# Kernel optimization log

Hardware: AMD Instinct MI355X
Metric: run time of the kernel (lower is better)

The kernel has to match this reference:

```python
import jax, jax.numpy as jnp
import numpy as np

USER = 100000
ITEM = 100000
N = USER + ITEM          # total nodes
D = 64                   # latdim
DEG = 16                 # avg edges per user (before symmetrization)
L_GNN = 2                # args.gnn_layer
L_MLP = 2                # args.layer_mlp
EPS = 1e-5               # LayerNorm eps


def setup_inputs() -> dict:
    key = jax.random.key(0)
    k1, k2, k3, k4, k5 = jax.random.split(key, 5)
    # bipartite user->item edges, then symmetrize (bi_adj over N x N nodes)
    u = jax.random.randint(k1, (USER * DEG,), 0, USER)
    v = jax.random.randint(k2, (USER * DEG,), 0, ITEM) + USER
    rows = jnp.concatenate([u, v]).astype(jnp.int64)
    cols = jnp.concatenate([v, u]).astype(jnp.int64)
    # symmetric D^-1/2 A D^-1/2 normalization (matches _normalize_adj)
    deg = jnp.zeros((N,), jnp.float32).at[rows].add(1.0)
    vals = 1.0 / (jnp.sqrt(deg[rows]) * jnp.sqrt(deg[cols]))
    # xavier-uniform-ish initial embeddings (detached in the source)
    bound = float(np.sqrt(6.0 / (N + D)))
    ini_embeds = jax.random.uniform(k3, (N, D), jnp.float32, -bound, bound)
    # MLP params: L_MLP stacked Linear(latdim, latdim)
    wb = float(np.sqrt(6.0 / (D + D)))
    Ws = jax.random.uniform(k4, (L_MLP, D, D), jnp.float32, -wb, wb)
    bs = jnp.zeros((L_MLP, D), jnp.float32)
    gamma = jnp.ones((D,), jnp.float32)
    beta = jnp.zeros((D,), jnp.float32)
    return {"rows": rows, "cols": cols, "vals": vals, "ini_embeds": ini_embeds,
            "Ws": Ws, "bs": bs, "gamma": gamma, "beta": beta}


def reference(rows, cols, vals, ini_embeds, Ws, bs, gamma, beta):
    # UntrainedGCN.forward: multi-hop spmm propagation (concat=0, symetric=True)
    e = ini_embeds
    for _ in range(L_GNN):
        # spmm: out[r] += vals * e[c] for each edge (r, c)
        e = jax.ops.segment_sum(vals[:, None] * e[cols], rows, num_segments=N)
    # residual MLP: relu(Wx+b) + x per FeedForwardLayer
    for i in range(L_MLP):
        e = jax.nn.relu(e @ Ws[i].T + bs[i]) + e
    # LayerNorm over last dim
    mu = e.mean(-1, keepdims=True)
    xc = e - mu
    var = (xc * xc).mean(-1, keepdims=True)
    e = xc * jax.lax.rsqrt(var + EPS) * gamma + beta
    return e[:USER], e[USER:]
```

## Files before the change

### kernel.cpp

```cpp
#include <hip/hip_runtime.h>
#include <hip/hip_bf16.h>

#define NN      200000
#define D       64
#define NTILE   12500
#define BKT_SH  8
#define BKT_RW  256
#define NBKT    782
#define NCHUNK  128
#define L2CAP   6656
#define CPAD    16
#define RSENT   256

typedef __attribute__((ext_vector_type(8))) short short8;
typedef __attribute__((ext_vector_type(4))) float f32x4;

__device__ inline unsigned short f32_to_bf16_rne(float x) {
    unsigned u = __float_as_uint(x);
    unsigned r = u + 0x7FFFu + ((u >> 16) & 1u);
    return (unsigned short)(r >> 16);
}
__device__ inline float bf16_bits_to_f32(unsigned short h) {
    return __uint_as_float(((unsigned)h) << 16);
}
__device__ inline unsigned pack2_bf16_rne(float lo, float hi) {
    unsigned a = __float_as_uint(lo);
    unsigned b = __float_as_uint(hi);
    a = a + 0x7FFFu + ((a >> 16) & 1u);
    b = b + 0x7FFFu + ((b >> 16) & 1u);
    return (a >> 16) | (b & 0xFFFF0000u);
}
__device__ inline float bf_lo(unsigned u) { return __uint_as_float(u << 16); }
__device__ inline float bf_hi(unsigned u) { return __uint_as_float(u & 0xFFFF0000u); }

__global__ __launch_bounds__(256) void zero_f4(float4* __restrict__ p, int n4) {
    int i = blockIdx.x * blockDim.x + threadIdx.x;
    if (i < n4) p[i] = make_float4(0.f, 0.f, 0.f, 0.f);
}
__global__ __launch_bounds__(256) void zero_i(int* __restrict__ p, int n) {
    int i = blockIdx.x * blockDim.x + threadIdx.x;
    if (i < n) p[i] = 0;
}
__global__ __launch_bounds__(256) void cvt_bf16(const float2* __restrict__ in,
                                                unsigned* __restrict__ out, int n) {
    int stride = gridDim.x * blockDim.x;
    for (int i = blockIdx.x * blockDim.x + threadIdx.x; i < n; i += stride) {
        float2 v = in[i];
        out[i] = pack2_bf16_rne(v.x, v.y);
    }
}

template <int ALIGN>
__global__ __launch_bounds__(1024) void bkt_count(const int* __restrict__ rows,
                                                  int* __restrict__ tot_p,
                                                  int E, int epb) {
    __shared__ int h[NBKT];
    int t = threadIdx.x;
    for (int i = t; i < NBKT; i += 1024) h[i] = 0;
    __syncthreads();
    int start = blockIdx.x * epb;
    int end   = min(E, start + epb);
    for (int e = start + t; e < end; e += 1024)
        atomicAdd(&h[rows[e] >> BKT_SH], 1);
    __syncthreads();
    for (int i = t; i < NBKT; i += 1024) {
        int c   = h[i];
        int res = (c + ALIGN - 1) & ~(ALIGN - 1);
        if (res) atomicAdd(&tot_p[i * CPAD], res);
    }
}

__global__ __launch_bounds__(1024) void bkt_scan(const int* __restrict__ tot_p,
                                                 int* __restrict__ bktstart,
                                                 int* __restrict__ cursor_p) {
    __shared__ int s[1024];
    int t = threadIdx.x;
    int v = (t < NBKT) ? tot_p[t * CPAD] : 0;
    s[t] = v;
    __syncthreads();
    #pragma unroll
    for (int d = 1; d < 1024; d <<= 1) {
        int a = (t >= d) ? s[t - d] : 0;
        __syncthreads();
        s[t] += a;
        __syncthreads();
    }
    if (t < NBKT) {
        int ex = s[t] - v;
        bktstart[t] = ex;
        cursor_p[t * CPAD] = ex;
    }
    if (t == 0) bktstart[NBKT] = s[1023];
}

template <int ALIGN>
__global__ __launch_bounds__(1024) void scatter_l1(const int* __restrict__ rows,
                                                   const int* __restrict__ cols,
                                                   const float* __restrict__ vals,
                                                   int* __restrict__ cursor_p,
                                                   int2* __restrict__ packed,
                                                   int E, int epb) {
    __shared__ int h[NBKT];
    __shared__ int base[NBKT];
    int t = threadIdx.x;
    for (int i = t; i < NBKT; i += 1024) h[i] = 0;
    __syncthreads();
    int start = blockIdx.x * epb;
    int end   = min(E, start + epb);
    for (int e = start + t; e < end; e += 1024)
        atomicAdd(&h[rows[e] >> BKT_SH], 1);
    __syncthreads();
    for (int i = t; i < NBKT; i += 1024) {
        int c   = h[i];
        int res = (c + ALIGN - 1) & ~(ALIGN - 1);
        int b0  = res ? atomicAdd(&cursor_p[i * CPAD], res) : 0;
        base[i] = b0;
        for (int j = c; j < res; ++j)
            packed[b0 + j] = make_int2(RSENT << 18, 0);
        h[i] = 0;
    }
    __syncthreads();
    for (int e = start + t; e < end; e += 1024) {
        int r = rows[e];
        int b = r >> BKT_SH;
        int p = base[b] + atomicAdd(&h[b], 1);
        packed[p] = make_int2(cols[e] | ((r & (BKT_RW - 1)) << 18),
                              __float_as_int(vals[e]));
    }
}

__global__ __launch_bounds__(256) void sort_l2(const int* __restrict__ bktstart,
                                               int2* __restrict__ packed,
                                               int* __restrict__ rp,
                                               int* __restrict__ rpe) {
    __shared__ int2 sm[L2CAP];
    __shared__ int  cnt[BKT_RW];
    __shared__ int  cur[BKT_RW];
    int b = blockIdx.x;
    int s = bktstart[b];
    int e = bktstart[b + 1];
    int n = e - s;
    if (n > L2CAP) n = L2CAP;
    int t = threadIdx.x;
    cnt[t] = 0;
    __syncthreads();
    for (int i = t; i < n; i += 256) {
        int2 v = packed[s + i];
        sm[i] = v;
        int r = (v.x >> 18) & 0x1FF;
        if (r < BKT_RW) atomicAdd(&cnt[r], 1);
    }
    __syncthreads();
    #pragma unroll
    for (int d = 1; d < BKT_RW; d <<= 1) {
        int a = (t >= d) ? cnt[t - d] : 0;
        __syncthreads();
        cnt[t] += a;
        __syncthreads();
    }
    {
        int ex = t ? cnt[t - 1] : 0;
        cur[t] = ex;
        int g = (b << BKT_SH) + t;
        if (g < NN) { rp[g] = s + ex; rpe[g] = s + cnt[t]; }
    }
    __syncthreads();
    for (int i = t; i < n; i += 256) {
        int2 v = sm[i];
        int  r = (v.x >> 18) & 0x1FF;
        if (r < BKT_RW) {
            int p = atomicAdd(&cur[r], 1);
            packed[s + p] = make_int2(v.x & 0x3FFFF, v.y);
        }
    }
}

template <int OUT_BF16>
__global__ __launch_bounds__(256) void spmm_q(const int* __restrict__ rp,
                                              const int* __restrict__ rpe,
                                              const int2* __restrict__ packed,
                                              const uint2* __restrict__ ein,
                                              uint2* __restrict__ out_bf,
                                              float4* __restrict__ out_f32, int n) {
    int wave = (blockIdx.x * 256 + threadIdx.x) >> 6;
    int lane = threadIdx.x & 63;
    int l    = lane & 15;
    int row  = wave * 4 + (lane >> 4);

    float ax = 0.f, ay = 0.f, az = 0.f, aw = 0.f;
    int s = 0, e = 0;
    if (row < n) { s = rp[row]; e = rpe[row]; }

    for (int base = s; base < e; base += 16) {
        int cnt = e - base; if (cnt > 16) cnt = 16;
        int2 ev = make_int2(0, 0);
        if (l < cnt) ev = packed[base + l];
        int k = 0;
        for (; k + 4 <= cnt; k += 4) {
            int   c0 = __shfl(ev.x, k,     16), c1 = __shfl(ev.x, k + 1, 16);
            int   c2 = __shfl(ev.x, k + 2, 16), c3 = __shfl(ev.x, k + 3, 16);
            float v0 = __int_as_float(__shfl(ev.y, k,     16));
            float v1 = __int_as_float(__shfl(ev.y, k + 1, 16));
            float v2 = __int_as_float(__shfl(ev.y, k + 2, 16));
            float v3 = __int_as_float(__shfl(ev.y, k + 3, 16));
            uint2 g0 = ein[c0 * 16 + l];
            uint2 g1 = ein[c1 * 16 + l];
            uint2 g2 = ein[c2 * 16 + l];
            uint2 g3 = ein[c3 * 16 + l];
            ax += v0 * bf_lo(g0.x); ay += v0 * bf_hi(g0.x);
            az += v0 * bf_lo(g0.y); aw += v0 * bf_hi(g0.y);
            ax += v1 * bf_lo(g1.x); ay += v1 * bf_hi(g1.x);
            az += v1 * bf_lo(g1.y); aw += v1 * bf_hi(g1.y);
            ax += v2 * bf_lo(g2.x); ay += v2 * bf_hi(g2.x);
            az += v2 * bf_lo(g2.y); aw += v2 * bf_hi(g2.y);
            ax += v3 * bf_lo(g3.x); ay += v3 * bf_hi(g3.x);
            az += v3 * bf_lo(g3.y); aw += v3 * bf_hi(g3.y);
        }
        for (; k + 2 <= cnt; k += 2) {
            int   c0 = __shfl(ev.x, k, 16), c1 = __shfl(ev.x, k + 1, 16);
            float v0 = __int_as_float(__shfl(ev.y, k,     16));
            float v1 = __int_as_float(__shfl(ev.y, k + 1, 16));
            uint2 g0 = ein[c0 * 16 + l];
            uint2 g1 = ein[c1 * 16 + l];
            ax += v0 * bf_lo(g0.x); ay += v0 * bf_hi(g0.x);
            az += v0 * bf_lo(g0.y); aw += v0 * bf_hi(g0.y);
            ax += v1 * bf_lo(g1.x); ay += v1 * bf_hi(g1.x);
            az += v1 * bf_lo(g1.y); aw += v1 * bf_hi(g1.y);
        }
        if (k < cnt) {
            int   c0 = __shfl(ev.x, k, 16);
            float v0 = __int_as_float(__shfl(ev.y, k, 16));
            uint2 g0 = ein[c0 * 16 + l];
            ax += v0 * bf_lo(g0.x); ay += v0 * bf_hi(g0.x);
            az += v0 * bf_lo(g0.y); aw += v0 * bf_hi(g0.y);
        }
    }
    if (row < n) {
        if (OUT_BF16) {
            out_bf[(size_t)row * 16 + l] =
                make_uint2(pack2_bf16_rne(ax, ay), pack2_bf16_rne(az, aw));
        } else {
            out_f32[(size_t)row * 16 + l] = make_float4(ax, ay, az, aw);
        }
    }
}

__global__ __launch_bounds__(256) void spmm_scatter(const int* __restrict__ rows,
                                                    const int* __restrict__ cols,
                                                    const float* __restrict__ vals,
                                                    const float* __restrict__ ein,
                                                    float* __restrict__ eout, int E) {
    int gid  = blockIdx.x * blockDim.x + threadIdx.x;
    int wid  = gid >> 6;
    int lane = threadIdx.x & 63;
    int nw   = (gridDim.x * blockDim.x) >> 6;
    for (int e = wid; e < E; e += nw) {
        int   r = rows[e];
        int   c = cols[e];
        float v = vals[e];
        float x = ein[(size_t)c * D + lane];
        unsafeAtomicAdd(&eout[(size_t)r * D + lane], v * x);
    }
}

__global__ __launch_bounds__(256) void mlp_mfma(float* __restrict__ e,
                                                const float* __restrict__ Ws,
                                                const float* __restrict__ bs,
                                                const float* __restrict__ gamma,
                                                const float* __restrict__ beta) {
    __shared__ float xp[4][16][68];
    int t  = threadIdx.x;
    int wv = t >> 6;
    int fr = t & 15;
    int fq = (t & 63) >> 4;

    short8 wh[2][4][2], wl[2][4][2];
    #pragma unroll
    for (int l = 0; l < 2; ++l)
        #pragma unroll
        for (int nt = 0; nt < 4; ++nt)
            #pragma unroll
            for (int kk = 0; kk < 2; ++kk) {
                const float* src = Ws + l * 4096 + (nt * 16 + fr) * 64 + kk * 32 + fq * 8;
                float4 a = *(const float4*)src;
                float4 b = *(const float4*)(src + 4);
                float v[8] = {a.x, a.y, a.z, a.w, b.x, b.y, b.z, b.w};
                short8 H, L;
                #pragma unroll
                for (int j = 0; j < 8; ++j) {
                    unsigned short hh = f32_to_bf16_rne(v[j]);
                    H[j] = hh;
                    L[j] = f32_to_bf16_rne(v[j] - bf16_bits_to_f32(hh));
                }
                wh[l][nt][kk] = H;
                wl[l][nt][kk] = L;
            }
    float bia0[4], bia1[4], gam[4], bet[4];
    #pragma unroll
    for (int nt = 0; nt < 4; ++nt) {
        bia0[nt] = bs[nt * 16 + fr];
        bia1[nt] = bs[64 + nt * 16 + fr];
        gam[nt]  = gamma[nt * 16 + fr];
        bet[nt]  = beta[nt * 16 + fr];
    }

    int wgid = blockIdx.x * 4 + wv;
    int nwv  = gridDim.x * 4;
    for (int tile = wgid; tile < NTILE; tile += nwv) {
        float* base = e + (size_t)tile * 16 * D;

        short8 xh[2], xl[2];
        #pragma unroll
        for (int kk = 0; kk < 2; ++kk) {
            const float* s = base + fr * D + kk * 32 + fq * 8;
            float4 a = *(const float4*)s;
            float4 b = *(const float4*)(s + 4);
            float v[8] = {a.x, a.y, a.z, a.w, b.x, b.y, b.z, b.w};
            #pragma unroll
            for (int j = 0; j < 8; ++j) {
                unsigned short hh = f32_to_bf16_rne(v[j]);
                xh[kk][j] = hh;
                xl[kk][j] = f32_to_bf16_rne(v[j] - bf16_bits_to_f32(hh));
            }
        }
        float xr[4][4];
        #pragma unroll
        for (int nt = 0; nt < 4; ++nt)
            #pragma unroll
            for (int j = 0; j < 4; ++j)
                xr[nt][j] = base[(fq * 4 + j) * D + nt * 16 + fr];

        f32x4 acc[4];
        #pragma unroll
        for (int nt = 0; nt < 4; ++nt) {
            acc[nt] = f32x4{bia0[nt], bia0[nt], bia0[nt], bia0[nt]};
            #pragma unroll
            for (int kk = 0; kk < 2; ++kk) {
                acc[nt] = __builtin_amdgcn_mfma_f32_16x16x32_bf16(xl[kk], wh[0][nt][kk], acc[nt], 0, 0, 0);
                acc[nt] = __builtin_amdgcn_mfma_f32_16x16x32_bf16(xh[kk], wl[0][nt][kk], acc[nt], 0, 0, 0);
                acc[nt] = __builtin_amdgcn_mfma_f32_16x16x32_bf16(xh[kk], wh[0][nt][kk], acc[nt], 0, 0, 0);
            }
        }
        float y1[4][4];
        #pragma unroll
        for (int nt = 0; nt < 4; ++nt)
            #pragma unroll
            for (int j = 0; j < 4; ++j) {
                y1[nt][j] = fmaxf(acc[nt][j], 0.f) + xr[nt][j];
                xp[wv][fq * 4 + j][nt * 16 + fr] = y1[nt][j];
            }

        #pragma unroll
        for (int kk = 0; kk < 2; ++kk) {
            const float* s = &xp[wv][fr][kk * 32 + fq * 8];
            float4 a = *(const float4*)s;
            float4 b = *(const float4*)(s + 4);
            float v[8] = {a.x, a.y, a.z, a.w, b.x, b.y, b.z, b.w};
            #pragma unroll
            for (int j = 0; j < 8; ++j) {
                unsigned short hh = f32_to_bf16_rne(v[j]);
                xh[kk][j] = hh;
                xl[kk][j] = f32_to_bf16_rne(v[j] - bf16_bits_to_f32(hh));
            }
        }

        #pragma unroll
        for (int nt = 0; nt < 4; ++nt) {
            acc[nt] = f32x4{bia1[nt], bia1[nt], bia1[nt], bia1[nt]};
            #pragma unroll
            for (int kk = 0; kk < 2; ++kk) {
                acc[nt] = __builtin_amdgcn_mfma_f32_16x16x32_bf16(xl[kk], wh[1][nt][kk], acc[nt], 0, 0, 0);
                acc[nt] = __builtin_amdgcn_mfma_f32_16x16x32_bf16(xh[kk], wl[1][nt][kk], acc[nt], 0, 0, 0);
                acc[nt] = __builtin_amdgcn_mfma_f32_16x16x32_bf16(xh[kk], wh[1][nt][kk], acc[nt], 0, 0, 0);
            }
        }
        float y2[4][4];
        #pragma unroll
        for (int nt = 0; nt < 4; ++nt)
            #pragma unroll
            for (int j = 0; j < 4; ++j)
                y2[nt][j] = fmaxf(acc[nt][j], 0.f) + y1[nt][j];

        float sm[4], sq[4];
        #pragma unroll
        for (int j = 0; j < 4; ++j) {
            float s0 = 0.f, q0 = 0.f;
            #pragma unroll
            for (int nt = 0; nt < 4; ++nt) { s0 += y2[nt][j]; q0 += y2[nt][j] * y2[nt][j]; }
            sm[j] = s0; sq[j] = q0;
        }
        #pragma unroll
        for (int off = 1; off < 16; off <<= 1) {
            #pragma unroll
            for (int j = 0; j < 4; ++j) {
                sm[j] += __shfl_xor(sm[j], off);
                sq[j] += __shfl_xor(sq[j], off);
            }
        }
        #pragma unroll
        for (int j = 0; j < 4; ++j) {
            float mu  = sm[j] * (1.f / 64.f);
            float var = sq[j] * (1.f / 64.f) - mu * mu;
            float rs  = rsqrtf(var + 1e-5f);
            #pragma unroll
            for (int nt = 0; nt < 4; ++nt)
                base[(fq * 4 + j) * D + nt * 16 + fr] =
                    (y2[nt][j] - mu) * rs * gam[nt] + bet[nt];
        }
    }
}

template <int ALIGN>
static void run_csr(const int* rows, const int* cols, const float* vals,
                    const float* ini, float* out, char* w, int E, size_t packed_cap,
                    hipStream_t stream) {
    size_t inibf_b  = (size_t)NN * 32 * 4;
    size_t e1bf_b   = inibf_b;
    size_t packed_b = packed_cap * 8;
    size_t rp_b     = (((size_t)NN + 1) * 4 + 63) & ~(size_t)63;
    size_t rpe_b    = (ALIGN > 1) ? rp_b : 0;
    size_t bsrt_b   = (((size_t)NBKT + 1) * 4 + 63) & ~(size_t)63;
    size_t pad_b    = (size_t)NBKT * CPAD * 4;

    unsigned* ini_bf   = (unsigned*)w;  w += inibf_b;
    unsigned* e1_bf    = (unsigned*)w;  w += e1bf_b;
    int2*     packed   = (int2*)w;      w += packed_b;
    int*      rp       = (int*)w;       w += rp_b;
    int*      rpe      = (ALIGN > 1) ? (int*)w : rp + 1;  w += rpe_b;
    int*      bktstart = (int*)w;       w += bsrt_b;
    int*      tot_p    = (int*)w;       w += pad_b;
    int*      cursor_p = (int*)w;

    int epb = (E + NCHUNK - 1) / NCHUNK;
    cvt_bf16<<<2048, 256, 0, stream>>>((const float2*)ini, ini_bf, NN * 32);
    zero_i<<<(NBKT * CPAD + 255) / 256, 256, 0, stream>>>(tot_p, NBKT * CPAD);
    bkt_count<ALIGN><<<NCHUNK, 1024, 0, stream>>>(rows, tot_p, E, epb);
    bkt_scan<<<1, 1024, 0, stream>>>(tot_p, bktstart, cursor_p);
    scatter_l1<ALIGN><<<NCHUNK, 1024, 0, stream>>>(rows, cols, vals, cursor_p, packed, E, epb);
    sort_l2<<<NBKT, 256, 0, stream>>>(bktstart, packed, rp, rpe);

    int waves = (NN + 3) / 4;
    int blocks = (waves + 3) / 4;
    spmm_q<1><<<blocks, 256, 0, stream>>>(rp, rpe, packed, (const uint2*)ini_bf,
                                          (uint2*)e1_bf, nullptr, NN);
    spmm_q<0><<<blocks, 256, 0, stream>>>(rp, rpe, packed, (const uint2*)e1_bf,
                                          nullptr, (float4*)out, NN);
}

extern "C" void kernel_launch(void* const* d_in, const int* in_sizes, int n_in,
                              void* d_out, int out_size, void* d_ws, size_t ws_size,
                              hipStream_t stream) {
    const int*   rows  = (const int*)d_in[0];
    const int*   cols  = (const int*)d_in[1];
    const float* vals  = (const float*)d_in[2];
    const float* ini   = (const float*)d_in[3];
    const float* Ws    = (const float*)d_in[4];
    const float* bs    = (const float*)d_in[5];
    const float* gamma = (const float*)d_in[6];
    const float* beta  = (const float*)d_in[7];
    float* out = (float*)d_out;
    int E = in_sizes[0];

    size_t inibf_b = (size_t)NN * 32 * 4;
    size_t rp_b    = (((size_t)NN + 1) * 4 + 63) & ~(size_t)63;
    size_t bsrt_b  = (((size_t)NBKT + 1) * 4 + 63) & ~(size_t)63;
    size_t pad_b   = (size_t)NBKT * CPAD * 4;
    size_t cap8    = (size_t)E + (size_t)NBKT * NCHUNK * 7;
    size_t cap1    = (size_t)E;
    size_t need8   = 2 * inibf_b + cap8 * 8 + 2 * rp_b + bsrt_b + 2 * pad_b;
    size_t need1   = 2 * inibf_b + cap1 * 8 + rp_b + bsrt_b + 2 * pad_b;

    if (ws_size >= need8) {
        run_csr<8>(rows, cols, vals, ini, out, (char*)d_ws, E, cap8, stream);
    } else if (ws_size >= need1) {
        run_csr<1>(rows, cols, vals, ini, out, (char*)d_ws, E, cap1, stream);
    } else {
        float* e1 = (float*)d_ws;
        int n4 = out_size / 4;
        int zb = (n4 + 255) / 256;
        zero_f4<<<zb, 256, 0, stream>>>((float4*)e1,  n4);
        zero_f4<<<zb, 256, 0, stream>>>((float4*)out, n4);
        spmm_scatter<<<12800, 256, 0, stream>>>(rows, cols, vals, ini, e1, E);
        spmm_scatter<<<12800, 256, 0, stream>>>(rows, cols, vals, e1, out, E);
    }

    mlp_mfma<<<1563, 256, 0, stream>>>(out, Ws, bs, gamma, beta);
}
```

Baseline: 278.2 us.

## Restructure MLP kernel with LDS-staged tiles and single-bf16 weights

Replaces the MLP kernel. Weights are converted once per block to single bf16 and kept in LDS instead of hi/lo split registers, which drops one MFMA per k-step. Each 16-row tile is staged through LDS with coalesced float4 loads and stores, so the strided global reads and writes go away. The grid shrinks to 512 blocks and NCHUNK doubles for the CSR path. Dropping the weight low part lowers matmul precision, so the result may drift from the fp32 reference.

```diff
diff --git a/kernel.cpp b/kernel.cpp
--- a/kernel.cpp
+++ b/kernel.cpp
@@ -7,12 +7,13 @@
 #define BKT_SH  8
 #define BKT_RW  256
 #define NBKT    782
-#define NCHUNK  128
+#define NCHUNK  256
 #define L2CAP   6656
 #define CPAD    16
 #define RSENT   256
 
 typedef __attribute__((ext_vector_type(8))) short short8;
+typedef __attribute__((ext_vector_type(4))) short short4v;
 typedef __attribute__((ext_vector_type(4))) float f32x4;
 
 __device__ inline unsigned short f32_to_bf16_rne(float x) {
@@ -263,132 +264,100 @@
     }
 }
 
-__global__ __launch_bounds__(256) void mlp_mfma(float* __restrict__ e,
-                                                const float* __restrict__ Ws,
-                                                const float* __restrict__ bs,
-                                                const float* __restrict__ gamma,
-                                                const float* __restrict__ beta) {
-    __shared__ float xp[4][16][68];
-    int t  = threadIdx.x;
-    int wv = t >> 6;
-    int fr = t & 15;
-    int fq = (t & 63) >> 4;
-
-    short8 wh[2][4][2], wl[2][4][2];
+__global__ __launch_bounds__(256) void mlp_v2(float* __restrict__ e,
+                                              const float* __restrict__ Ws,
+                                              const float* __restrict__ bs,
+                                              const float* __restrict__ gamma,
+                                              const float* __restrict__ beta) {
+    __shared__ unsigned short wlds[2][64][72];
+    __shared__ float tb[4][16][68];
+
+    int t    = threadIdx.x;
+    int wv   = t >> 6;
+    int lane = t & 63;
+    int fr   = t & 15;
+    int fq   = lane >> 4;
+
+    for (int i = t * 4; i < 2 * 64 * 64; i += 1024) {
+        float4 f = *(const float4*)(Ws + i);
+        int l = i >> 12, r = (i >> 6) & 63, c = i & 63;
+        short4v s4;
+        s4[0] = (short)f32_to_bf16_rne(f.x);
+        s4[1] = (short)f32_to_bf16_rne(f.y);
+        s4[2] = (short)f32_to_bf16_rne(f.z);
+        s4[3] = (short)f32_to_bf16_rne(f.w);
+        *(short4v*)&wlds[l][r][c] = s4;
+    }
+    __syncthreads();
+
+    float bia[2][4], gam[4], bet[4];
     #pragma unroll
-    for (int l = 0; l < 2; ++l)
-        #pragma unroll
-        for (int nt = 0; nt < 4; ++nt)
+    for (int nt = 0; nt < 4; ++nt) {
+        bia[0][nt] = bs[nt * 16 + fr];
+        bia[1][nt] = bs[64 + nt * 16 + fr];
+        gam[nt]    = gamma[nt * 16 + fr];
+        bet[nt]    = beta[nt * 16 + fr];
+    }
+
+    float (*tw)[68] = tb[wv];
+
+    for (int tile = blockIdx.x * 4 + wv; tile < NTILE; tile += gridDim.x * 4) {
+        float* base = e + (size_t)tile * 1024;
+
+        #pragma unroll
+        for (int it = 0; it < 4; ++it) {
+            int idx = it * 256 + lane * 4;
+            *(float4*)&tw[idx >> 6][idx & 63] = *(const float4*)(base + idx);
+        }
+
+        #pragma unroll
+        for (int l = 0; l < 2; ++l) {
+            short8 xh[2], xl[2];
             #pragma unroll
             for (int kk = 0; kk < 2; ++kk) {
-                const float* src = Ws + l * 4096 + (nt * 16 + fr) * 64 + kk * 32 + fq * 8;
-                float4 a = *(const float4*)src;
-                float4 b = *(const float4*)(src + 4);
-                float v[8] = {a.x, a.y, a.z, a.w, b.x, b.y, b.z, b.w};
-                short8 H, L;
+                const float* s = &tw[fr][kk * 32 + fq * 8];
+                float4 a = *(const float4*)s;
+                float4 b4 = *(const float4*)(s + 4);
+                float v[8] = {a.x, a.y, a.z, a.w, b4.x, b4.y, b4.z, b4.w};
                 #pragma unroll
                 for (int j = 0; j < 8; ++j) {
                     unsigned short hh = f32_to_bf16_rne(v[j]);
-                    H[j] = hh;
-                    L[j] = f32_to_bf16_rne(v[j] - bf16_bits_to_f32(hh));
+                    xh[kk][j] = (short)hh;
+                    xl[kk][j] = (short)f32_to_bf16_rne(v[j] - bf16_bits_to_f32(hh));
                 }
-                wh[l][nt][kk] = H;
-                wl[l][nt][kk] = L;
             }
-    float bia0[4], bia1[4], gam[4], bet[4];
-    #pragma unroll
-    for (int nt = 0; nt < 4; ++nt) {
-        bia0[nt] = bs[nt * 16 + fr];
-        bia1[nt] = bs[64 + nt * 16 + fr];
-        gam[nt]  = gamma[nt * 16 + fr];
-        bet[nt]  = beta[nt * 16 + fr];
-    }
-
-    int wgid = blockIdx.x * 4 + wv;
-    int nwv  = gridDim.x * 4;
-    for (int tile = wgid; tile < NTILE; tile += nwv) {
-        float* base = e + (size_t)tile * 16 * D;
-
-        short8 xh[2], xl[2];
-        #pragma unroll
-        for (int kk = 0; kk < 2; ++kk) {
-            const float* s = base + fr * D + kk * 32 + fq * 8;
-            float4 a = *(const float4*)s;
-            float4 b = *(const float4*)(s + 4);
-            float v[8] = {a.x, a.y, a.z, a.w, b.x, b.y, b.z, b.w};
-            #pragma unroll
-            for (int j = 0; j < 8; ++j) {
-                unsigned short hh = f32_to_bf16_rne(v[j]);
-                xh[kk][j] = hh;
-                xl[kk][j] = f32_to_bf16_rne(v[j] - bf16_bits_to_f32(hh));
+            f32x4 acc[4];
+            #pragma unroll
+            for (int nt = 0; nt < 4; ++nt) {
+                float bb = bia[l][nt];
+                acc[nt] = f32x4{bb, bb, bb, bb};
+                #pragma unroll
+                for (int kk = 0; kk < 2; ++kk) {
+                    short8 w8 = *(const short8*)&wlds[l][nt * 16 + fr][kk * 32 + fq * 8];
+                    acc[nt] = __builtin_amdgcn_mfma_f32_16x16x32_bf16(xl[kk], w8, acc[nt], 0, 0, 0);
+                    acc[nt] = __builtin_amdgcn_mfma_f32_16x16x32_bf16(xh[kk], w8, acc[nt], 0, 0, 0);
+                }
             }
-        }
-        float xr[4][4];
+            #pragma unroll
+            for (int nt = 0; nt < 4; ++nt)
+                #pragma unroll
+                for (int j = 0; j < 4; ++j) {
+                    float* cell = &tw[fq * 4 + j][nt * 16 + fr];
+                    *cell = fmaxf(acc[nt][j], 0.f) + *cell;
+                }
+        }
+
+        float y2[4][4], sm[4], sq[4];
+        #pragma unroll
+        for (int j = 0; j < 4; ++j) { sm[j] = 0.f; sq[j] = 0.f; }
         #pragma unroll
         for (int nt = 0; nt < 4; ++nt)
             #pragma unroll
-            for (int j = 0; j < 4; ++j)
-                xr[nt][j] = base[(fq * 4 + j) * D + nt * 16 + fr];
-
-        f32x4 acc[4];
-        #pragma unroll
-        for (int nt = 0; nt < 4; ++nt) {
-            acc[nt] = f32x4{bia0[nt], bia0[nt], bia0[nt], bia0[nt]};
-            #pragma unroll
-            for (int kk = 0; kk < 2; ++kk) {
-                acc[nt] = __builtin_amdgcn_mfma_f32_16x16x32_bf16(xl[kk], wh[0][nt][kk], acc[nt], 0, 0, 0);
-                acc[nt] = __builtin_amdgcn_mfma_f32_16x16x32_bf16(xh[kk], wl[0][nt][kk], acc[nt], 0, 0, 0);
-                acc[nt] = __builtin_amdgcn_mfma_f32_16x16x32_bf16(xh[kk], wh[0][nt][kk], acc[nt], 0, 0, 0);
+            for (int j = 0; j < 4; ++j) {
+                float v = tw[fq * 4 + j][nt * 16 + fr];
+                y2[nt][j] = v;
+                sm[j] += v; sq[j] += v * v;
             }
-        }
-        float y1[4][4];
-        #pragma unroll
-        for (int nt = 0; nt < 4; ++nt)
-            #pragma unroll
-            for (int j = 0; j < 4; ++j) {
-                y1[nt][j] = fmaxf(acc[nt][j], 0.f) + xr[nt][j];
-                xp[wv][fq * 4 + j][nt * 16 + fr] = y1[nt][j];
-            }
-
-        #pragma unroll
-        for (int kk = 0; kk < 2; ++kk) {
-            const float* s = &xp[wv][fr][kk * 32 + fq * 8];
-            float4 a = *(const float4*)s;
-            float4 b = *(const float4*)(s + 4);
-            float v[8] = {a.x, a.y, a.z, a.w, b.x, b.y, b.z, b.w};
-            #pragma unroll
-            for (int j = 0; j < 8; ++j) {
-                unsigned short hh = f32_to_bf16_rne(v[j]);
-                xh[kk][j] = hh;
-                xl[kk][j] = f32_to_bf16_rne(v[j] - bf16_bits_to_f32(hh));
-            }
-        }
-
-        #pragma unroll
-        for (int nt = 0; nt < 4; ++nt) {
-            acc[nt] = f32x4{bia1[nt], bia1[nt], bia1[nt], bia1[nt]};
-            #pragma unroll
-            for (int kk = 0; kk < 2; ++kk) {
-                acc[nt] = __builtin_amdgcn_mfma_f32_16x16x32_bf16(xl[kk], wh[1][nt][kk], acc[nt], 0, 0, 0);
-                acc[nt] = __builtin_amdgcn_mfma_f32_16x16x32_bf16(xh[kk], wl[1][nt][kk], acc[nt], 0, 0, 0);
-                acc[nt] = __builtin_amdgcn_mfma_f32_16x16x32_bf16(xh[kk], wh[1][nt][kk], acc[nt], 0, 0, 0);
-            }
-        }
-        float y2[4][4];
-        #pragma unroll
-        for (int nt = 0; nt < 4; ++nt)
-            #pragma unroll
-            for (int j = 0; j < 4; ++j)
-                y2[nt][j] = fmaxf(acc[nt][j], 0.f) + y1[nt][j];
-
-        float sm[4], sq[4];
-        #pragma unroll
-        for (int j = 0; j < 4; ++j) {
-            float s0 = 0.f, q0 = 0.f;
-            #pragma unroll
-            for (int nt = 0; nt < 4; ++nt) { s0 += y2[nt][j]; q0 += y2[nt][j] * y2[nt][j]; }
-            sm[j] = s0; sq[j] = q0;
-        }
         #pragma unroll
         for (int off = 1; off < 16; off <<= 1) {
             #pragma unroll
@@ -404,8 +373,13 @@
             float rs  = rsqrtf(var + 1e-5f);
             #pragma unroll
             for (int nt = 0; nt < 4; ++nt)
-                base[(fq * 4 + j) * D + nt * 16 + fr] =
-                    (y2[nt][j] - mu) * rs * gam[nt] + bet[nt];
+                tw[fq * 4 + j][nt * 16 + fr] = (y2[nt][j] - mu) * rs * gam[nt] + bet[nt];
+        }
+
+        #pragma unroll
+        for (int it = 0; it < 4; ++it) {
+            int idx = it * 256 + lane * 4;
+            *(float4*)(base + idx) = *(const float4*)&tw[idx >> 6][idx & 63];
         }
     }
 }
@@ -484,5 +458,5 @@
         spmm_scatter<<<12800, 256, 0, stream>>>(rows, cols, vals, e1, out, E);
     }
 
-    mlp_mfma<<<1563, 256, 0, stream>>>(out, Ws, bs, gamma, beta);
-}
+    mlp_v2<<<512, 256, 0, stream>>>(out, Ws, bs, gamma, beta);
+}
```

Measured after the change: 234.0 us. 1.19x faster.
